# Kernel optimization log

Measured on AMD Instinct MI355X. Metric: run time of the kernel, lower is better.

## Reference

```python
import jax, jax.numpy as jnp
import numpy as np

N_QUBITS = 8
DIM = 2 ** N_QUBITS  # 256
N_CYCLES = 4
BATCH = 8192

# ---- gate matrices (work for scalar or batched [B] angles) ----

def _rz(t):
    e0 = jnp.exp(-0.5j * t.astype(jnp.complex64))
    e1 = jnp.exp(0.5j * t.astype(jnp.complex64))
    z = jnp.zeros_like(e0)
    return jnp.stack([jnp.stack([e0, z], -1), jnp.stack([z, e1], -1)], -2)


def _ry(t):
    c = jnp.cos(t / 2)
    s = jnp.sin(t / 2)
    m = jnp.stack([jnp.stack([c, -s], -1), jnp.stack([s, c], -1)], -2)
    return m.astype(jnp.complex64)


def _u3(t, p, l):
    ct = jnp.cos(t / 2).astype(jnp.complex64)
    st = jnp.sin(t / 2).astype(jnp.complex64)
    ep = jnp.exp(1j * p.astype(jnp.complex64))
    el = jnp.exp(1j * l.astype(jnp.complex64))
    return jnp.stack([jnp.stack([ct, -el * st], -1),
                      jnp.stack([ep * st, ep * el * ct], -1)], -2)

# ---- state-vector gate application (wire 0 = most significant, torchquantum convention) ----

def apply_1q(psi, U, w):
    B = psi.shape[0]
    p = psi.reshape(B, 2 ** w, 2, -1)
    if U.ndim == 3:
        p = jnp.einsum('bij,bajc->baic', U, p)
    else:
        p = jnp.einsum('ij,bajc->baic', U, p)
    return p.reshape(B, DIM)


def apply_cnot(psi, c, t):
    p = psi.reshape((-1,) + (2,) * N_QUBITS)
    c_ax, t_ax = c + 1, t + 1
    p0 = jax.lax.index_in_dim(p, 0, c_ax, keepdims=True)
    p1 = jnp.flip(jax.lax.index_in_dim(p, 1, c_ax, keepdims=True), axis=t_ax)
    return jnp.concatenate([p0, p1], axis=c_ax).reshape(-1, DIM)


def expval_z(psi, w):
    pr = (psi.real ** 2 + psi.imag ** 2).reshape(psi.shape[0], 2 ** w, 2, -1)
    pr = pr.sum(axis=(1, 3))
    return pr[:, 0] - pr[:, 1]


def conv_block(psi, hi, lo, rza, rzb, rzc, rya, ryb):
    # rz(hi); cnot(hi,lo); rz(lo); ry(hi); cnot(lo,hi); ry(hi); cnot(hi,lo); rz(lo)
    psi = apply_1q(psi, _rz(rza), hi)
    psi = apply_cnot(psi, hi, lo)
    psi = apply_1q(psi, _rz(rzb), lo)
    psi = apply_1q(psi, _ry(rya), hi)
    psi = apply_cnot(psi, lo, hi)
    psi = apply_1q(psi, _ry(ryb), hi)
    psi = apply_cnot(psi, hi, lo)
    psi = apply_1q(psi, _rz(rzc), lo)
    return psi


def _forward(theta, phi, rz_angles, ry_angles, u3_params, w1, b1, w2, b2):
    B = theta.shape[0]
    psi = jnp.zeros((B, DIM), jnp.complex64).at[:, 0].set(1.0)
    # circuit builder (assumed): per cycle RY(theta), RZ(phi) on every wire + CNOT ring
    Ury = _ry(theta)  # [B,2,2]
    Urz = _rz(phi)
    for _ in range(N_CYCLES):
        for w in range(N_QUBITS):
            psi = apply_1q(psi, Ury, w)
        for w in range(N_QUBITS):
            psi = apply_1q(psi, Urz, w)
        for w in range(N_QUBITS):
            psi = apply_cnot(psi, w, (w + 1) % N_QUBITS)
    # conv layer 1: pairs (1,0),(3,2),(5,4),(7,6) using rz1-12, ry1-8
    for i, (hi, lo) in enumerate([(1, 0), (3, 2), (5, 4), (7, 6)]):
        psi = conv_block(psi, hi, lo, rz_angles[3 * i], rz_angles[3 * i + 1],
                         rz_angles[3 * i + 2], ry_angles[2 * i], ry_angles[2 * i + 1])
    # intermediate expvals on [0,2,4,6] are computed-and-discarded in the original (non-collapsing): no-op
    for j, w in enumerate([1, 3, 5, 7]):
        psi = apply_1q(psi, _u3(u3_params[j, 0], u3_params[j, 1], u3_params[j, 2]), w)
    # conv layer 2: pairs (3,1),(7,5),(5,3) using rz13-21, ry9-14
    for k, (hi, lo) in enumerate([(3, 1), (7, 5), (5, 3)]):
        i = 4 + k
        psi = conv_block(psi, hi, lo, rz_angles[3 * i], rz_angles[3 * i + 1],
                         rz_angles[3 * i + 2], ry_angles[2 * i], ry_angles[2 * i + 1])
    # discarded expvals on [1,5]: no-op
    psi = apply_1q(psi, _u3(u3_params[4, 0], u3_params[4, 1], u3_params[4, 2]), 3)
    psi = apply_1q(psi, _u3(u3_params[5, 0], u3_params[5, 1], u3_params[5, 2]), 7)
    x = jnp.stack([expval_z(psi, 3), expval_z(psi, 7)], axis=-1)  # [B,2] real
    h = jnp.tanh(x @ w1.T + b1)
    y = h @ w2.T + b2
    return jax.nn.sigmoid(y)  # [B,1]


def setup_inputs() -> dict:
    key = jax.random.key(0)
    ks = jax.random.split(key, 9)
    return {
        'theta': jax.random.normal(ks[0], (BATCH,), jnp.float32),
        'phi': jax.random.normal(ks[1], (BATCH,), jnp.float32),
        'rz_angles': jax.random.normal(ks[2], (21,), jnp.float32),
        'ry_angles': jax.random.normal(ks[3], (14,), jnp.float32),
        'u3_params': jax.random.normal(ks[4], (6, 3), jnp.float32),
        'w1': jax.random.normal(ks[5], (10, 2), jnp.float32) * 0.5,
        'b1': jax.random.normal(ks[6], (10,), jnp.float32) * 0.1,
        'w2': jax.random.normal(ks[7], (1, 10), jnp.float32) * 0.3,
        'b2': jax.random.normal(ks[8], (1,), jnp.float32) * 0.1,
    }


def reference(theta, phi, rz_angles, ry_angles, u3_params, w1, b1, w2, b2):
    return _forward(theta, phi, rz_angles, ry_angles, u3_params, w1, b1, w2, b2)
```

## Files before the change

kernel.cpp:

```cpp
#include <hip/hip_runtime.h>
#include <math.h>


constexpr int NREG = 8;

typedef float v2f __attribute__((ext_vector_type(2)));

__device__ __forceinline__ v2f vfma(v2f a, v2f b, v2f c) {
  return __builtin_elementwise_fma(a, b, c);
}
__device__ __forceinline__ v2f splat(float x) { return (v2f){x, x}; }

template<int MASK>
__device__ __forceinline__ float lxor(float x) {
  int xi = __float_as_int(x);
  int r;
  if constexpr (MASK == 1)      r = __builtin_amdgcn_mov_dpp(xi, 0xB1, 0xF, 0xF, true);
  else if constexpr (MASK == 2) r = __builtin_amdgcn_mov_dpp(xi, 0x4E, 0xF, 0xF, true);
  else                          r = __builtin_amdgcn_ds_swizzle(xi, (MASK << 10) | 0x1F);
  return __int_as_float(r);
}

template<int MASK>
__device__ __forceinline__ v2f lxor2(v2f v) {
  v2f r;
  r.x = lxor<MASK>(v.x);
  r.y = lxor<MASK>(v.y);
  return r;
}

struct State {
  v2f a[NREG];
};

template<int P>
__device__ __forceinline__ void ry_gate(State& st, float c, float s, int L) {
  if constexpr (P <= 2) {
    constexpr int m = 1 << P;
    #pragma unroll
    for (int r0 = 0; r0 < NREG; ++r0) {
      if (r0 & m) continue;
      const int r1 = r0 | m;
      v2f a0 = st.a[r0], a1 = st.a[r1];
      st.a[r0] = vfma(splat(-s), a1, splat(c) * a0);
      st.a[r1] = vfma(splat( s), a0, splat(c) * a1);
    }
  } else {
    constexpr int m = 1 << (P - 3);
    float ss = ((L >> (P - 3)) & 1) ? s : -s;
    #pragma unroll
    for (int r = 0; r < NREG; ++r) {
      v2f b = lxor2<m>(st.a[r]);
      st.a[r] = vfma(splat(ss), b, splat(c) * st.a[r]);
    }
  }
}

template<int P>
__device__ __forceinline__ void rz_gate(State& st, float cz, float sz, int L) {
  if constexpr (P <= 2) {
    #pragma unroll
    for (int r = 0; r < NREG; ++r) {
      float sg = ((r >> P) & 1) ? sz : -sz;
      v2f v = st.a[r];
      st.a[r] = vfma((v2f){-sg, sg}, v.yx, splat(cz) * v);
    }
  } else {
    float sg = ((L >> (P - 3)) & 1) ? sz : -sz;
    #pragma unroll
    for (int r = 0; r < NREG; ++r) {
      v2f v = st.a[r];
      st.a[r] = vfma((v2f){-sg, sg}, v.yx, splat(cz) * v);
    }
  }
}

template<int PC, int PT>
__device__ __forceinline__ void cnot_gate(State& st, int L) {
  if constexpr (PT <= 2) {
    constexpr int mt = 1 << PT;
    if constexpr (PC <= 2) {
      constexpr int mc = 1 << PC;
      #pragma unroll
      for (int r0 = 0; r0 < NREG; ++r0) {
        if (!(r0 & mc) || (r0 & mt)) continue;
        const int r1 = r0 | mt;
        v2f t = st.a[r0]; st.a[r0] = st.a[r1]; st.a[r1] = t;
      }
    } else {
      bool cb = (L >> (PC - 3)) & 1;
      #pragma unroll
      for (int r0 = 0; r0 < NREG; ++r0) {
        if (r0 & mt) continue;
        const int r1 = r0 | mt;
        v2f a0 = st.a[r0], a1 = st.a[r1];
        st.a[r0] = cb ? a1 : a0;
        st.a[r1] = cb ? a0 : a1;
      }
    }
  } else {
    constexpr int mt = 1 << (PT - 3);
    if constexpr (PC <= 2) {
      constexpr int mc = 1 << PC;
      #pragma unroll
      for (int r = 0; r < NREG; ++r) {
        if (!(r & mc)) continue;
        st.a[r] = lxor2<mt>(st.a[r]);
      }
    } else {
      bool cb = (L >> (PC - 3)) & 1;
      #pragma unroll
      for (int r = 0; r < NREG; ++r) {
        v2f b = lxor2<mt>(st.a[r]);
        st.a[r] = cb ? b : st.a[r];
      }
    }
  }
}

__device__ __forceinline__ v2f cmac(v2f t, float ur, float ui, v2f v) {
  t = vfma(splat(ur), v, t);
  t = vfma((v2f){-ui, ui}, v.yx, t);
  return t;
}

template<int P>
__device__ __forceinline__ void u3_gate(State& st, const float* u, int L) {
  float u00r=u[0],u00i=u[1],u01r=u[2],u01i=u[3],u10r=u[4],u10i=u[5],u11r=u[6],u11i=u[7];
  if constexpr (P <= 2) {
    constexpr int m = 1 << P;
    #pragma unroll
    for (int r0 = 0; r0 < NREG; ++r0) {
      if (r0 & m) continue;
      const int r1 = r0 | m;
      v2f a0 = st.a[r0], a1 = st.a[r1];
      v2f t0 = splat(u00r) * a0;
      t0 = vfma((v2f){-u00i, u00i}, a0.yx, t0);
      t0 = cmac(t0, u01r, u01i, a1);
      v2f t1 = splat(u10r) * a0;
      t1 = vfma((v2f){-u10i, u10i}, a0.yx, t1);
      t1 = cmac(t1, u11r, u11i, a1);
      st.a[r0] = t0;
      st.a[r1] = t1;
    }
  } else {
    constexpr int m = 1 << (P - 3);
    bool b = (L >> (P - 3)) & 1;
    float xr = b ? u11r : u00r, xi = b ? u11i : u00i;
    float yr = b ? u10r : u01r, yi = b ? u10i : u01i;
    #pragma unroll
    for (int r = 0; r < NREG; ++r) {
      v2f p = lxor2<m>(st.a[r]);
      v2f v = st.a[r];
      v2f t = splat(xr) * v;
      t = vfma((v2f){-xi, xi}, v.yx, t);
      t = cmac(t, yr, yi, p);
      st.a[r] = t;
    }
  }
}

template<int PH, int PL>
__device__ __forceinline__ void conv_block(State& st, int L,
    float crza,float srza, float crzb,float srzb, float crzc,float srzc,
    float crya,float srya, float cryb,float sryb) {
  rz_gate<PH>(st, crza, srza, L);
  cnot_gate<PH, PL>(st, L);
  rz_gate<PL>(st, crzb, srzb, L);
  ry_gate<PH>(st, crya, srya, L);
  cnot_gate<PL, PH>(st, L);
  ry_gate<PH>(st, cryb, sryb, L);
  cnot_gate<PH, PL>(st, L);
  rz_gate<PL>(st, crzc, srzc, L);
}

__global__ __launch_bounds__(256, 4) void qcnn_kernel(
    const float* __restrict__ theta, const float* __restrict__ phi,
    const float* __restrict__ rz_a, const float* __restrict__ ry_a,
    const float* __restrict__ u3_p,
    const float* __restrict__ w1, const float* __restrict__ b1,
    const float* __restrict__ w2, const float* __restrict__ b2,
    float* __restrict__ out, int B) {
  __shared__ float s_rz[21][2];
  __shared__ float s_ry[14][2];
  __shared__ float s_u3[6][8];
  __shared__ float s_w1[20];
  __shared__ float s_b1[10];
  __shared__ float s_w2[10];
  __shared__ float s_b2[1];

  const int tid = threadIdx.x;
  if (tid < 21) {
    float s, c; sincosf(0.5f * rz_a[tid], &s, &c);
    s_rz[tid][0] = c; s_rz[tid][1] = s;
  } else if (tid >= 32 && tid < 46) {
    int j = tid - 32;
    float s, c; sincosf(0.5f * ry_a[j], &s, &c);
    s_ry[j][0] = c; s_ry[j][1] = s;
  } else if (tid >= 64 && tid < 70) {
    int j = tid - 64;
    float t = u3_p[3*j], p = u3_p[3*j+1], l = u3_p[3*j+2];
    float st_, ct, sp, cp, sl, cl;
    sincosf(0.5f*t, &st_, &ct);
    sincosf(p, &sp, &cp);
    sincosf(l, &sl, &cl);
    s_u3[j][0] = ct;       s_u3[j][1] = 0.f;
    s_u3[j][2] = -cl*st_;  s_u3[j][3] = -sl*st_;
    s_u3[j][4] = cp*st_;   s_u3[j][5] = sp*st_;
    float eplr = cp*cl - sp*sl, epli = sp*cl + cp*sl;
    s_u3[j][6] = eplr*ct;  s_u3[j][7] = epli*ct;
  } else if (tid >= 96 && tid < 116) {
    s_w1[tid - 96] = w1[tid - 96];
  } else if (tid >= 128 && tid < 138) {
    s_b1[tid - 128] = b1[tid - 128];
  } else if (tid >= 160 && tid < 170) {
    s_w2[tid - 160] = w2[tid - 160];
  } else if (tid == 192) {
    s_b2[0] = b2[0];
  }
  __syncthreads();

  const int L = tid & 31;
  const int g = (blockIdx.x * blockDim.x + tid) >> 5;
  if (g < B) {
    float th = theta[g], ph = phi[g];
    float cth, sth; sincosf(0.5f*th, &sth, &cth);
    float cph, sph; sincosf(0.5f*ph, &sph, &cph);

    State st;
    #pragma unroll
    for (int r = 0; r < NREG; ++r) st.a[r] = (v2f){0.f, 0.f};
    st.a[0].x = (L == 0) ? 1.f : 0.f;

    #pragma unroll 1
    for (int cyc = 0; cyc < 4; ++cyc) {
      ry_gate<7>(st, cth, sth, L);
      ry_gate<6>(st, cth, sth, L);
      ry_gate<5>(st, cth, sth, L);
      ry_gate<4>(st, cth, sth, L);
      ry_gate<3>(st, cth, sth, L);
      ry_gate<2>(st, cth, sth, L);
      ry_gate<1>(st, cth, sth, L);
      ry_gate<0>(st, cth, sth, L);
      rz_gate<7>(st, cph, sph, L);
      rz_gate<6>(st, cph, sph, L);
      rz_gate<5>(st, cph, sph, L);
      rz_gate<4>(st, cph, sph, L);
      rz_gate<3>(st, cph, sph, L);
      rz_gate<2>(st, cph, sph, L);
      rz_gate<1>(st, cph, sph, L);
      rz_gate<0>(st, cph, sph, L);
      cnot_gate<7,6>(st, L);
      cnot_gate<6,5>(st, L);
      cnot_gate<5,4>(st, L);
      cnot_gate<4,3>(st, L);
      cnot_gate<3,2>(st, L);
      cnot_gate<2,1>(st, L);
      cnot_gate<1,0>(st, L);
      cnot_gate<0,7>(st, L);
    }

    #define CONVB(PH, PL, i) conv_block<PH, PL>(st, L, \
        s_rz[3*(i)][0],   s_rz[3*(i)][1],   \
        s_rz[3*(i)+1][0], s_rz[3*(i)+1][1], \
        s_rz[3*(i)+2][0], s_rz[3*(i)+2][1], \
        s_ry[2*(i)][0],   s_ry[2*(i)][1],   \
        s_ry[2*(i)+1][0], s_ry[2*(i)+1][1])
    CONVB(6, 7, 0);
    CONVB(4, 5, 1);
    CONVB(2, 3, 2);
    CONVB(0, 1, 3);

    u3_gate<6>(st, s_u3[0], L);
    u3_gate<4>(st, s_u3[1], L);
    u3_gate<2>(st, s_u3[2], L);
    u3_gate<0>(st, s_u3[3], L);

    CONVB(4, 6, 4);
    CONVB(0, 2, 5);
    CONVB(2, 4, 6);
    #undef CONVB

    u3_gate<4>(st, s_u3[4], L);
    u3_gate<0>(st, s_u3[5], L);

    float s3 = 0.f, s7 = 0.f;
    #pragma unroll
    for (int r = 0; r < NREG; ++r) {
      v2f sq = st.a[r] * st.a[r];
      float p = sq.x + sq.y;
      s3 += p;
      s7 += (r & 1) ? -p : p;
    }
    if ((L >> 1) & 1) s3 = -s3;
    s3 += lxor<1>(s3);  s7 += lxor<1>(s7);
    s3 += lxor<2>(s3);  s7 += lxor<2>(s7);
    s3 += lxor<4>(s3);  s7 += lxor<4>(s7);
    s3 += lxor<8>(s3);  s7 += lxor<8>(s7);
    s3 += lxor<16>(s3); s7 += lxor<16>(s7);

    float y = s_b2[0];
    #pragma unroll
    for (int j = 0; j < 10; ++j) {
      float h = tanhf(fmaf(s3, s_w1[2*j], fmaf(s7, s_w1[2*j+1], s_b1[j])));
      y = fmaf(h, s_w2[j], y);
    }
    float res = 1.f / (1.f + expf(-y));
    if (L == 0) out[g] = res;
  }
}

extern "C" void kernel_launch(void* const* d_in, const int* in_sizes, int n_in,
                              void* d_out, int out_size, void* d_ws, size_t ws_size,
                              hipStream_t stream) {
  const float* theta = (const float*)d_in[0];
  const float* phi   = (const float*)d_in[1];
  const float* rz_a  = (const float*)d_in[2];
  const float* ry_a  = (const float*)d_in[3];
  const float* u3_p  = (const float*)d_in[4];
  const float* w1    = (const float*)d_in[5];
  const float* b1    = (const float*)d_in[6];
  const float* w2    = (const float*)d_in[7];
  const float* b2    = (const float*)d_in[8];
  float* out = (float*)d_out;
  const int B = in_sizes[0];
  const int threads = 256;
  const int blocks = (B * 32 + threads - 1) / threads;
  hipLaunchKernelGGL(qcnn_kernel, dim3(blocks), dim3(threads), 0, stream,
                     theta, phi, rz_a, ry_a, u3_p, w1, b1, w2, b2, out, B);
}
```

Measured before the change: 31.92 us.

## Process two batch elements per 32-lane group to raise ILP

Each 32-lane group now simulates two independent state vectors (two batch samples) interleaved in registers, halving the grid size and giving every gate two independent dependency chains. The aim is to hide DPP/swizzle and FMA latency and to amortize the per-group setup, parameter reads and reduction. In exchange register use doubles and launch bounds drop to 2 blocks per CU, which lowers occupancy and leaves fewer blocks to spread across CUs.

New measurement: 34.63 us. 1.08x slower.

```diff
diff --git a/kernel.cpp b/kernel.cpp
--- a/kernel.cpp
+++ b/kernel.cpp
@@ -29,54 +29,85 @@
   return r;
 }
 
-struct State {
-  v2f a[NREG];
+struct St2 {
+  v2f a[2][NREG];
 };
 
+
 template<int P>
-__device__ __forceinline__ void ry_gate(State& st, float c, float s, int L) {
+__device__ __forceinline__ void ry2(St2& st, float c0, float s0, float c1, float s1, int L) {
+  const float cc[2] = {c0, c1};
+  const float ss[2] = {s0, s1};
   if constexpr (P <= 2) {
     constexpr int m = 1 << P;
     #pragma unroll
     for (int r0 = 0; r0 < NREG; ++r0) {
       if (r0 & m) continue;
       const int r1 = r0 | m;
-      v2f a0 = st.a[r0], a1 = st.a[r1];
-      st.a[r0] = vfma(splat(-s), a1, splat(c) * a0);
-      st.a[r1] = vfma(splat( s), a0, splat(c) * a1);
+      #pragma unroll
+      for (int e = 0; e < 2; ++e) {
+        v2f a0 = st.a[e][r0], a1 = st.a[e][r1];
+        st.a[e][r0] = vfma(splat(-ss[e]), a1, splat(cc[e]) * a0);
+        st.a[e][r1] = vfma(splat( ss[e]), a0, splat(cc[e]) * a1);
+      }
     }
   } else {
     constexpr int m = 1 << (P - 3);
-    float ss = ((L >> (P - 3)) & 1) ? s : -s;
+    const bool bit = (L >> (P - 3)) & 1;
+    const float sg[2] = {bit ? s0 : -s0, bit ? s1 : -s1};
     #pragma unroll
     for (int r = 0; r < NREG; ++r) {
-      v2f b = lxor2<m>(st.a[r]);
-      st.a[r] = vfma(splat(ss), b, splat(c) * st.a[r]);
+      #pragma unroll
+      for (int e = 0; e < 2; ++e) {
+        v2f b = lxor2<m>(st.a[e][r]);
+        st.a[e][r] = vfma(splat(sg[e]), b, splat(cc[e]) * st.a[e][r]);
+      }
     }
   }
 }
 
 template<int P>
-__device__ __forceinline__ void rz_gate(State& st, float cz, float sz, int L) {
+__device__ __forceinline__ void rz2(St2& st, float c0, float s0, float c1, float s1, int L) {
+  const float cc[2] = {c0, c1};
+  const float ss[2] = {s0, s1};
   if constexpr (P <= 2) {
     #pragma unroll
     for (int r = 0; r < NREG; ++r) {
-      float sg = ((r >> P) & 1) ? sz : -sz;
-      v2f v = st.a[r];
-      st.a[r] = vfma((v2f){-sg, sg}, v.yx, splat(cz) * v);
+      const bool bit = (r >> P) & 1;
+      #pragma unroll
+      for (int e = 0; e < 2; ++e) {
+        float sg = bit ? ss[e] : -ss[e];
+        v2f v = st.a[e][r];
+        st.a[e][r] = vfma((v2f){-sg, sg}, v.yx, splat(cc[e]) * v);
+      }
     }
   } else {
-    float sg = ((L >> (P - 3)) & 1) ? sz : -sz;
+    const bool bit = (L >> (P - 3)) & 1;
+    const float sg[2] = {bit ? s0 : -s0, bit ? s1 : -s1};
     #pragma unroll
     for (int r = 0; r < NREG; ++r) {
-      v2f v = st.a[r];
-      st.a[r] = vfma((v2f){-sg, sg}, v.yx, splat(cz) * v);
-    }
-  }
+      #pragma unroll
+      for (int e = 0; e < 2; ++e) {
+        v2f v = st.a[e][r];
+        st.a[e][r] = vfma((v2f){-sg[e], sg[e]}, v.yx, splat(cc[e]) * v);
+      }
+    }
+  }
+}
+
+
+template<int P>
+__device__ __forceinline__ void ry_s(St2& st, float c, float s, int L) {
+  ry2<P>(st, c, s, c, s, L);
+}
+
+template<int P>
+__device__ __forceinline__ void rz_s(St2& st, float cz, float sz, int L) {
+  rz2<P>(st, cz, sz, cz, sz, L);
 }
 
 template<int PC, int PT>
-__device__ __forceinline__ void cnot_gate(State& st, int L) {
+__device__ __forceinline__ void cnot2(St2& st, int L) {
   if constexpr (PT <= 2) {
     constexpr int mt = 1 << PT;
     if constexpr (PC <= 2) {
@@ -85,17 +116,23 @@
       for (int r0 = 0; r0 < NREG; ++r0) {
         if (!(r0 & mc) || (r0 & mt)) continue;
         const int r1 = r0 | mt;
-        v2f t = st.a[r0]; st.a[r0] = st.a[r1]; st.a[r1] = t;
+        #pragma unroll
+        for (int e = 0; e < 2; ++e) {
+          v2f t = st.a[e][r0]; st.a[e][r0] = st.a[e][r1]; st.a[e][r1] = t;
+        }
       }
     } else {
-      bool cb = (L >> (PC - 3)) & 1;
+      const bool cb = (L >> (PC - 3)) & 1;
       #pragma unroll
       for (int r0 = 0; r0 < NREG; ++r0) {
         if (r0 & mt) continue;
         const int r1 = r0 | mt;
-        v2f a0 = st.a[r0], a1 = st.a[r1];
-        st.a[r0] = cb ? a1 : a0;
-        st.a[r1] = cb ? a0 : a1;
+        #pragma unroll
+        for (int e = 0; e < 2; ++e) {
+          v2f a0 = st.a[e][r0], a1 = st.a[e][r1];
+          st.a[e][r0] = cb ? a1 : a0;
+          st.a[e][r1] = cb ? a0 : a1;
+        }
       }
     }
   } else {
@@ -105,14 +142,18 @@
       #pragma unroll
       for (int r = 0; r < NREG; ++r) {
         if (!(r & mc)) continue;
-        st.a[r] = lxor2<mt>(st.a[r]);
+        #pragma unroll
+        for (int e = 0; e < 2; ++e) st.a[e][r] = lxor2<mt>(st.a[e][r]);
       }
     } else {
-      bool cb = (L >> (PC - 3)) & 1;
+      const bool cb = (L >> (PC - 3)) & 1;
       #pragma unroll
       for (int r = 0; r < NREG; ++r) {
-        v2f b = lxor2<mt>(st.a[r]);
-        st.a[r] = cb ? b : st.a[r];
+        #pragma unroll
+        for (int e = 0; e < 2; ++e) {
+          v2f b = lxor2<mt>(st.a[e][r]);
+          st.a[e][r] = cb ? b : st.a[e][r];
+        }
       }
     }
   }
@@ -125,7 +166,7 @@
 }
 
 template<int P>
-__device__ __forceinline__ void u3_gate(State& st, const float* u, int L) {
+__device__ __forceinline__ void u3_s(St2& st, const float* u, int L) {
   float u00r=u[0],u00i=u[1],u01r=u[2],u01i=u[3],u10r=u[4],u10i=u[5],u11r=u[6],u11i=u[7];
   if constexpr (P <= 2) {
     constexpr int m = 1 << P;
@@ -133,48 +174,54 @@
     for (int r0 = 0; r0 < NREG; ++r0) {
       if (r0 & m) continue;
       const int r1 = r0 | m;
-      v2f a0 = st.a[r0], a1 = st.a[r1];
-      v2f t0 = splat(u00r) * a0;
-      t0 = vfma((v2f){-u00i, u00i}, a0.yx, t0);
-      t0 = cmac(t0, u01r, u01i, a1);
-      v2f t1 = splat(u10r) * a0;
-      t1 = vfma((v2f){-u10i, u10i}, a0.yx, t1);
-      t1 = cmac(t1, u11r, u11i, a1);
-      st.a[r0] = t0;
-      st.a[r1] = t1;
+      #pragma unroll
+      for (int e = 0; e < 2; ++e) {
+        v2f a0 = st.a[e][r0], a1 = st.a[e][r1];
+        v2f t0 = splat(u00r) * a0;
+        t0 = vfma((v2f){-u00i, u00i}, a0.yx, t0);
+        t0 = cmac(t0, u01r, u01i, a1);
+        v2f t1 = splat(u10r) * a0;
+        t1 = vfma((v2f){-u10i, u10i}, a0.yx, t1);
+        t1 = cmac(t1, u11r, u11i, a1);
+        st.a[e][r0] = t0;
+        st.a[e][r1] = t1;
+      }
     }
   } else {
     constexpr int m = 1 << (P - 3);
-    bool b = (L >> (P - 3)) & 1;
-    float xr = b ? u11r : u00r, xi = b ? u11i : u00i;
-    float yr = b ? u10r : u01r, yi = b ? u10i : u01i;
+    const bool b = (L >> (P - 3)) & 1;
+    const float xr = b ? u11r : u00r, xi = b ? u11i : u00i;
+    const float yr = b ? u10r : u01r, yi = b ? u10i : u01i;
     #pragma unroll
     for (int r = 0; r < NREG; ++r) {
-      v2f p = lxor2<m>(st.a[r]);
-      v2f v = st.a[r];
-      v2f t = splat(xr) * v;
-      t = vfma((v2f){-xi, xi}, v.yx, t);
-      t = cmac(t, yr, yi, p);
-      st.a[r] = t;
+      #pragma unroll
+      for (int e = 0; e < 2; ++e) {
+        v2f p = lxor2<m>(st.a[e][r]);
+        v2f v = st.a[e][r];
+        v2f t = splat(xr) * v;
+        t = vfma((v2f){-xi, xi}, v.yx, t);
+        t = cmac(t, yr, yi, p);
+        st.a[e][r] = t;
+      }
     }
   }
 }
 
 template<int PH, int PL>
-__device__ __forceinline__ void conv_block(State& st, int L,
+__device__ __forceinline__ void conv_block(St2& st, int L,
     float crza,float srza, float crzb,float srzb, float crzc,float srzc,
     float crya,float srya, float cryb,float sryb) {
-  rz_gate<PH>(st, crza, srza, L);
-  cnot_gate<PH, PL>(st, L);
-  rz_gate<PL>(st, crzb, srzb, L);
-  ry_gate<PH>(st, crya, srya, L);
-  cnot_gate<PL, PH>(st, L);
-  ry_gate<PH>(st, cryb, sryb, L);
-  cnot_gate<PH, PL>(st, L);
-  rz_gate<PL>(st, crzc, srzc, L);
-}
-
-__global__ __launch_bounds__(256, 4) void qcnn_kernel(
+  rz_s<PH>(st, crza, srza, L);
+  cnot2<PH, PL>(st, L);
+  rz_s<PL>(st, crzb, srzb, L);
+  ry_s<PH>(st, crya, srya, L);
+  cnot2<PL, PH>(st, L);
+  ry_s<PH>(st, cryb, sryb, L);
+  cnot2<PH, PL>(st, L);
+  rz_s<PL>(st, crzc, srzc, L);
+}
+
+__global__ __launch_bounds__(256, 2) void qcnn_kernel(
     const float* __restrict__ theta, const float* __restrict__ phi,
     const float* __restrict__ rz_a, const float* __restrict__ ry_a,
     const float* __restrict__ u3_p,
@@ -221,43 +268,52 @@
   __syncthreads();
 
   const int L = tid & 31;
-  const int g = (blockIdx.x * blockDim.x + tid) >> 5;
-  if (g < B) {
-    float th = theta[g], ph = phi[g];
-    float cth, sth; sincosf(0.5f*th, &sth, &cth);
-    float cph, sph; sincosf(0.5f*ph, &sph, &cph);
-
-    State st;
-    #pragma unroll
-    for (int r = 0; r < NREG; ++r) st.a[r] = (v2f){0.f, 0.f};
-    st.a[0].x = (L == 0) ? 1.f : 0.f;
+  const int grp = (blockIdx.x * blockDim.x + tid) >> 5;
+  const int g0 = 2 * grp;
+  const int g1 = 2 * grp + 1;
+  if (g0 < B) {
+    const int g1r = (g1 < B) ? g1 : g0;
+    float th0 = theta[g0], ph0 = phi[g0];
+    float th1 = theta[g1r], ph1 = phi[g1r];
+    float cth0, sth0; sincosf(0.5f*th0, &sth0, &cth0);
+    float cth1, sth1; sincosf(0.5f*th1, &sth1, &cth1);
+    float cph0, sph0; sincosf(0.5f*ph0, &sph0, &cph0);
+    float cph1, sph1; sincosf(0.5f*ph1, &sph1, &cph1);
+
+    St2 st;
+    #pragma unroll
+    for (int e = 0; e < 2; ++e)
+      #pragma unroll
+      for (int r = 0; r < NREG; ++r) st.a[e][r] = (v2f){0.f, 0.f};
+    st.a[0][0].x = (L == 0) ? 1.f : 0.f;
+    st.a[1][0].x = (L == 0) ? 1.f : 0.f;
 
     #pragma unroll 1
     for (int cyc = 0; cyc < 4; ++cyc) {
-      ry_gate<7>(st, cth, sth, L);
-      ry_gate<6>(st, cth, sth, L);
-      ry_gate<5>(st, cth, sth, L);
-      ry_gate<4>(st, cth, sth, L);
-      ry_gate<3>(st, cth, sth, L);
-      ry_gate<2>(st, cth, sth, L);
-      ry_gate<1>(st, cth, sth, L);
-      ry_gate<0>(st, cth, sth, L);
-      rz_gate<7>(st, cph, sph, L);
-      rz_gate<6>(st, cph, sph, L);
-      rz_gate<5>(st, cph, sph, L);
-      rz_gate<4>(st, cph, sph, L);
-      rz_gate<3>(st, cph, sph, L);
-      rz_gate<2>(st, cph, sph, L);
-      rz_gate<1>(st, cph, sph, L);
-      rz_gate<0>(st, cph, sph, L);
-      cnot_gate<7,6>(st, L);
-      cnot_gate<6,5>(st, L);
-      cnot_gate<5,4>(st, L);
-      cnot_gate<4,3>(st, L);
-      cnot_gate<3,2>(st, L);
-      cnot_gate<2,1>(st, L);
-      cnot_gate<1,0>(st, L);
-      cnot_gate<0,7>(st, L);
+      ry2<7>(st, cth0, sth0, cth1, sth1, L);
+      ry2<6>(st, cth0, sth0, cth1, sth1, L);
+      ry2<5>(st, cth0, sth0, cth1, sth1, L);
+      ry2<4>(st, cth0, sth0, cth1, sth1, L);
+      ry2<3>(st, cth0, sth0, cth1, sth1, L);
+      ry2<2>(st, cth0, sth0, cth1, sth1, L);
+      ry2<1>(st, cth0, sth0, cth1, sth1, L);
+      ry2<0>(st, cth0, sth0, cth1, sth1, L);
+      rz2<7>(st, cph0, sph0, cph1, sph1, L);
+      rz2<6>(st, cph0, sph0, cph1, sph1, L);
+      rz2<5>(st, cph0, sph0, cph1, sph1, L);
+      rz2<4>(st, cph0, sph0, cph1, sph1, L);
+      rz2<3>(st, cph0, sph0, cph1, sph1, L);
+      rz2<2>(st, cph0, sph0, cph1, sph1, L);
+      rz2<1>(st, cph0, sph0, cph1, sph1, L);
+      rz2<0>(st, cph0, sph0, cph1, sph1, L);
+      cnot2<7,6>(st, L);
+      cnot2<6,5>(st, L);
+      cnot2<5,4>(st, L);
+      cnot2<4,3>(st, L);
+      cnot2<3,2>(st, L);
+      cnot2<2,1>(st, L);
+      cnot2<1,0>(st, L);
+      cnot2<0,7>(st, L);
     }
 
     #define CONVB(PH, PL, i) conv_block<PH, PL>(st, L, \
@@ -271,42 +327,56 @@
     CONVB(2, 3, 2);
     CONVB(0, 1, 3);
 
-    u3_gate<6>(st, s_u3[0], L);
-    u3_gate<4>(st, s_u3[1], L);
-    u3_gate<2>(st, s_u3[2], L);
-    u3_gate<0>(st, s_u3[3], L);
+    u3_s<6>(st, s_u3[0], L);
+    u3_s<4>(st, s_u3[1], L);
+    u3_s<2>(st, s_u3[2], L);
+    u3_s<0>(st, s_u3[3], L);
 
     CONVB(4, 6, 4);
     CONVB(0, 2, 5);
     CONVB(2, 4, 6);
     #undef CONVB
 
-    u3_gate<4>(st, s_u3[4], L);
-    u3_gate<0>(st, s_u3[5], L);
-
-    float s3 = 0.f, s7 = 0.f;
+    u3_s<4>(st, s_u3[4], L);
+    u3_s<0>(st, s_u3[5], L);
+
+    float s3[2] = {0.f, 0.f}, s7[2] = {0.f, 0.f};
     #pragma unroll
     for (int r = 0; r < NREG; ++r) {
-      v2f sq = st.a[r] * st.a[r];
-      float p = sq.x + sq.y;
-      s3 += p;
-      s7 += (r & 1) ? -p : p;
-    }
-    if ((L >> 1) & 1) s3 = -s3;
-    s3 += lxor<1>(s3);  s7 += lxor<1>(s7);
-    s3 += lxor<2>(s3);  s7 += lxor<2>(s7);
-    s3 += lxor<4>(s3);  s7 += lxor<4>(s7);
-    s3 += lxor<8>(s3);  s7 += lxor<8>(s7);
-    s3 += lxor<16>(s3); s7 += lxor<16>(s7);
-
-    float y = s_b2[0];
-    #pragma unroll
-    for (int j = 0; j < 10; ++j) {
-      float h = tanhf(fmaf(s3, s_w1[2*j], fmaf(s7, s_w1[2*j+1], s_b1[j])));
-      y = fmaf(h, s_w2[j], y);
-    }
-    float res = 1.f / (1.f + expf(-y));
-    if (L == 0) out[g] = res;
+      #pragma unroll
+      for (int e = 0; e < 2; ++e) {
+        v2f sq = st.a[e][r] * st.a[e][r];
+        float p = sq.x + sq.y;
+        s3[e] += p;
+        s7[e] += (r & 1) ? -p : p;
+      }
+    }
+    const bool neg3 = (L >> 1) & 1;
+    #pragma unroll
+    for (int e = 0; e < 2; ++e) {
+      if (neg3) s3[e] = -s3[e];
+      s3[e] += lxor<1>(s3[e]);  s7[e] += lxor<1>(s7[e]);
+      s3[e] += lxor<2>(s3[e]);  s7[e] += lxor<2>(s7[e]);
+      s3[e] += lxor<4>(s3[e]);  s7[e] += lxor<4>(s7[e]);
+      s3[e] += lxor<8>(s3[e]);  s7[e] += lxor<8>(s7[e]);
+      s3[e] += lxor<16>(s3[e]); s7[e] += lxor<16>(s7[e]);
+    }
+
+    float res[2];
+    #pragma unroll
+    for (int e = 0; e < 2; ++e) {
+      float y = s_b2[0];
+      #pragma unroll
+      for (int j = 0; j < 10; ++j) {
+        float h = tanhf(fmaf(s3[e], s_w1[2*j], fmaf(s7[e], s_w1[2*j+1], s_b1[j])));
+        y = fmaf(h, s_w2[j], y);
+      }
+      res[e] = 1.f / (1.f + expf(-y));
+    }
+    if (L == 0) {
+      out[g0] = res[0];
+      if (g1 < B) out[g1] = res[1];
+    }
   }
 }
 
@@ -324,8 +394,9 @@
   const float* b2    = (const float*)d_in[8];
   float* out = (float*)d_out;
   const int B = in_sizes[0];
+  const int ngrp = (B + 1) / 2;
   const int threads = 256;
-  const int blocks = (B * 32 + threads - 1) / threads;
+  const int blocks = (ngrp * 32 + threads - 1) / threads;
   hipLaunchKernelGGL(qcnn_kernel, dim3(blocks), dim3(threads), 0, stream,
                      theta, phi, rz_a, ry_a, u3_p, w1, b1, w2, b2, out, B);
 }
```

## Fuse each conv block plus trailing U3 into a precomputed 4x4 two-qubit unitary

Applied to the files above, without the earlier changes.

The gate-angle-only conv blocks and the U3 gates that follow them are collapsed into seven dense complex 4x4 matrices, built once per thread block by a few threads and kept in shared memory. Each sample's state then gets one two-qubit matrix application per block, using lane shuffles or register pairs depending on where the qubits live, in place of eight separate gates. This cuts the number of gate passes and shuffles in the tail of the circuit. In exchange, each 4x4 application does more complex multiply-adds and reads more values from shared memory.

Measured after the change: 39.31 us. 23.1% more time.

```diff
diff --git a/kernel.cpp b/kernel.cpp
--- a/kernel.cpp
+++ b/kernel.cpp
@@ -32,6 +32,7 @@
 struct State {
   v2f a[NREG];
 };
+
 
 template<int P>
 __device__ __forceinline__ void ry_gate(State& st, float c, float s, int L) {
@@ -118,60 +119,160 @@
   }
 }
 
-__device__ __forceinline__ v2f cmac(v2f t, float ur, float ui, v2f v) {
-  t = vfma(splat(ur), v, t);
-  t = vfma((v2f){-ui, ui}, v.yx, t);
+__device__ __forceinline__ v2f cmac(v2f t, v2f u, v2f v) {
+  t = vfma(splat(u.x), v, t);
+  t = vfma((v2f){-u.y, u.y}, v.yx, t);
   return t;
 }
 
-template<int P>
-__device__ __forceinline__ void u3_gate(State& st, const float* u, int L) {
-  float u00r=u[0],u00i=u[1],u01r=u[2],u01i=u[3],u10r=u[4],u10i=u[5],u11r=u[6],u11i=u[7];
-  if constexpr (P <= 2) {
-    constexpr int m = 1 << P;
-    #pragma unroll
-    for (int r0 = 0; r0 < NREG; ++r0) {
-      if (r0 & m) continue;
-      const int r1 = r0 | m;
-      v2f a0 = st.a[r0], a1 = st.a[r1];
-      v2f t0 = splat(u00r) * a0;
-      t0 = vfma((v2f){-u00i, u00i}, a0.yx, t0);
-      t0 = cmac(t0, u01r, u01i, a1);
-      v2f t1 = splat(u10r) * a0;
-      t1 = vfma((v2f){-u10i, u10i}, a0.yx, t1);
-      t1 = cmac(t1, u11r, u11i, a1);
-      st.a[r0] = t0;
-      st.a[r1] = t1;
-    }
+__device__ __forceinline__ v2f ld2(const float* p) {
+  return (v2f){p[0], p[1]};
+}
+
+
+template<int MH, int ML>
+__device__ __forceinline__ void apply_G_ll(State& st, const float* g, int L) {
+  const int bh = (L & MH) ? 1 : 0;
+  const int bl = (L & ML) ? 1 : 0;
+  const int row = (bh << 1) | bl;
+  const float* gr = g + row * 8;
+  const v2f cS = ld2(gr + 2 * row);
+  const v2f cL = ld2(gr + 2 * (row ^ 1));
+  const v2f cH = ld2(gr + 2 * (row ^ 2));
+  const v2f cB = ld2(gr + 2 * (row ^ 3));
+  #pragma unroll
+  for (int r = 0; r < NREG; ++r) {
+    v2f v = st.a[r];
+    v2f pl = lxor2<ML>(v);
+    v2f ph = lxor2<MH>(v);
+    v2f pb = lxor2<MH | ML>(v);
+    v2f t = (v2f){0.f, 0.f};
+    t = cmac(t, cS, v);
+    t = cmac(t, cL, pl);
+    t = cmac(t, cH, ph);
+    t = cmac(t, cB, pb);
+    st.a[r] = t;
+  }
+}
+
+template<int MHR, int MLR>
+__device__ __forceinline__ void apply_G_rr(State& st, const float* g) {
+  #pragma unroll
+  for (int base = 0; base < NREG; ++base) {
+    if (base & (MHR | MLR)) continue;
+    v2f in0 = st.a[base];
+    v2f in1 = st.a[base | MLR];
+    v2f in2 = st.a[base | MHR];
+    v2f in3 = st.a[base | MHR | MLR];
+    #pragma unroll
+    for (int i = 0; i < 4; ++i) {
+      v2f t = (v2f){0.f, 0.f};
+      t = cmac(t, ld2(g + i * 8 + 0), in0);
+      t = cmac(t, ld2(g + i * 8 + 2), in1);
+      t = cmac(t, ld2(g + i * 8 + 4), in2);
+      t = cmac(t, ld2(g + i * 8 + 6), in3);
+      st.a[base | ((i >> 1) ? MHR : 0) | ((i & 1) ? MLR : 0)] = (i == 0) ? t : t;
+      if (i == 0) st.a[base] = t;
+      else if (i == 1) st.a[base | MLR] = t;
+      else if (i == 2) st.a[base | MHR] = t;
+      else st.a[base | MHR | MLR] = t;
+    }
+  }
+}
+
+template<int MREG, int ML>
+__device__ __forceinline__ void apply_G_mx(State& st, const float* g, int L) {
+  const int bl = (L & ML) ? 1 : 0;
+  const int r0w = bl;
+  const int r1w = 2 + bl;
+  const float* g0 = g + r0w * 8;
+  const float* g1 = g + r1w * 8;
+  const v2f c0S = ld2(g0 + 2 * r0w),       c0L = ld2(g0 + 2 * (r0w ^ 1));
+  const v2f c0H = ld2(g0 + 2 * (r0w ^ 2)), c0B = ld2(g0 + 2 * (r0w ^ 3));
+  const v2f c1S = ld2(g1 + 2 * r1w),       c1L = ld2(g1 + 2 * (r1w ^ 1));
+  const v2f c1H = ld2(g1 + 2 * (r1w ^ 2)), c1B = ld2(g1 + 2 * (r1w ^ 3));
+  v2f x[NREG];
+  #pragma unroll
+  for (int r = 0; r < NREG; ++r) x[r] = lxor2<ML>(st.a[r]);
+  v2f o[NREG];
+  #pragma unroll
+  for (int r = 0; r < NREG; ++r) {
+    v2f t = (v2f){0.f, 0.f};
+    if (r & MREG) {
+      t = cmac(t, c1S, st.a[r]);
+      t = cmac(t, c1L, x[r]);
+      t = cmac(t, c1H, st.a[r ^ MREG]);
+      t = cmac(t, c1B, x[r ^ MREG]);
+    } else {
+      t = cmac(t, c0S, st.a[r]);
+      t = cmac(t, c0L, x[r]);
+      t = cmac(t, c0H, st.a[r ^ MREG]);
+      t = cmac(t, c0B, x[r ^ MREG]);
+    }
+    o[r] = t;
+  }
+  #pragma unroll
+  for (int r = 0; r < NREG; ++r) st.a[r] = o[r];
+}
+
+
+__device__ __forceinline__ void b_phase(float* cr, float* ci, int i, float pc, float ps) {
+  float r = cr[i] * pc - ci[i] * ps;
+  float m = cr[i] * ps + ci[i] * pc;
+  cr[i] = r; ci[i] = m;
+}
+__device__ __forceinline__ void b_rz_hi(float* cr, float* ci, float t) {
+  float s, c; sincosf(0.5f * t, &s, &c);
+  b_phase(cr, ci, 0, c, -s); b_phase(cr, ci, 1, c, -s);
+  b_phase(cr, ci, 2, c,  s); b_phase(cr, ci, 3, c,  s);
+}
+__device__ __forceinline__ void b_rz_lo(float* cr, float* ci, float t) {
+  float s, c; sincosf(0.5f * t, &s, &c);
+  b_phase(cr, ci, 0, c, -s); b_phase(cr, ci, 2, c, -s);
+  b_phase(cr, ci, 1, c,  s); b_phase(cr, ci, 3, c,  s);
+}
+__device__ __forceinline__ void b_ry_hi(float* cr, float* ci, float t) {
+  float s, c; sincosf(0.5f * t, &s, &c);
+  #pragma unroll
+  for (int lo = 0; lo < 2; ++lo) {
+    int i0 = lo, i1 = 2 + lo;
+    float n0r = c * cr[i0] - s * cr[i1], n0i = c * ci[i0] - s * ci[i1];
+    float n1r = s * cr[i0] + c * cr[i1], n1i = s * ci[i0] + c * ci[i1];
+    cr[i0] = n0r; ci[i0] = n0i; cr[i1] = n1r; ci[i1] = n1i;
+  }
+}
+__device__ __forceinline__ void b_swap(float* cr, float* ci, int i, int j) {
+  float t;
+  t = cr[i]; cr[i] = cr[j]; cr[j] = t;
+  t = ci[i]; ci[i] = ci[j]; ci[j] = t;
+}
+__device__ __forceinline__ void b_u2(float* cr, float* ci, int i0, int i1,
+    float u00r, float u00i, float u01r, float u01i,
+    float u10r, float u10i, float u11r, float u11i) {
+  float v0r = cr[i0], v0i = ci[i0], v1r = cr[i1], v1i = ci[i1];
+  cr[i0] = u00r*v0r - u00i*v0i + u01r*v1r - u01i*v1i;
+  ci[i0] = u00r*v0i + u00i*v0r + u01r*v1i + u01i*v1r;
+  cr[i1] = u10r*v0r - u10i*v0i + u11r*v1r - u11i*v1i;
+  ci[i1] = u10r*v0i + u10i*v0r + u11r*v1i + u11i*v1r;
+}
+__device__ __forceinline__ void b_u3(float* cr, float* ci, bool on_hi,
+                                     float t, float p, float l) {
+  float st_, ct, sp, cp, sl, cl;
+  sincosf(0.5f * t, &st_, &ct);
+  sincosf(p, &sp, &cp);
+  sincosf(l, &sl, &cl);
+  float u00r = ct,        u00i = 0.f;
+  float u01r = -cl * st_, u01i = -sl * st_;
+  float u10r = cp * st_,  u10i = sp * st_;
+  float eplr = cp * cl - sp * sl, epli = sp * cl + cp * sl;
+  float u11r = eplr * ct, u11i = epli * ct;
+  if (on_hi) {
+    b_u2(cr, ci, 0, 2, u00r,u00i,u01r,u01i,u10r,u10i,u11r,u11i);
+    b_u2(cr, ci, 1, 3, u00r,u00i,u01r,u01i,u10r,u10i,u11r,u11i);
   } else {
-    constexpr int m = 1 << (P - 3);
-    bool b = (L >> (P - 3)) & 1;
-    float xr = b ? u11r : u00r, xi = b ? u11i : u00i;
-    float yr = b ? u10r : u01r, yi = b ? u10i : u01i;
-    #pragma unroll
-    for (int r = 0; r < NREG; ++r) {
-      v2f p = lxor2<m>(st.a[r]);
-      v2f v = st.a[r];
-      v2f t = splat(xr) * v;
-      t = vfma((v2f){-xi, xi}, v.yx, t);
-      t = cmac(t, yr, yi, p);
-      st.a[r] = t;
-    }
-  }
-}
-
-template<int PH, int PL>
-__device__ __forceinline__ void conv_block(State& st, int L,
-    float crza,float srza, float crzb,float srzb, float crzc,float srzc,
-    float crya,float srya, float cryb,float sryb) {
-  rz_gate<PH>(st, crza, srza, L);
-  cnot_gate<PH, PL>(st, L);
-  rz_gate<PL>(st, crzb, srzb, L);
-  ry_gate<PH>(st, crya, srya, L);
-  cnot_gate<PL, PH>(st, L);
-  ry_gate<PH>(st, cryb, sryb, L);
-  cnot_gate<PH, PL>(st, L);
-  rz_gate<PL>(st, crzc, srzc, L);
+    b_u2(cr, ci, 0, 1, u00r,u00i,u01r,u01i,u10r,u10i,u11r,u11i);
+    b_u2(cr, ci, 2, 3, u00r,u00i,u01r,u01i,u10r,u10i,u11r,u11i);
+  }
 }
 
 __global__ __launch_bounds__(256, 4) void qcnn_kernel(
@@ -181,34 +282,37 @@
     const float* __restrict__ w1, const float* __restrict__ b1,
     const float* __restrict__ w2, const float* __restrict__ b2,
     float* __restrict__ out, int B) {
-  __shared__ float s_rz[21][2];
-  __shared__ float s_ry[14][2];
-  __shared__ float s_u3[6][8];
+  __shared__ float sG[7 * 32] __attribute__((aligned(16)));
   __shared__ float s_w1[20];
   __shared__ float s_b1[10];
   __shared__ float s_w2[10];
   __shared__ float s_b2[1];
 
   const int tid = threadIdx.x;
-  if (tid < 21) {
-    float s, c; sincosf(0.5f * rz_a[tid], &s, &c);
-    s_rz[tid][0] = c; s_rz[tid][1] = s;
-  } else if (tid >= 32 && tid < 46) {
-    int j = tid - 32;
-    float s, c; sincosf(0.5f * ry_a[j], &s, &c);
-    s_ry[j][0] = c; s_ry[j][1] = s;
-  } else if (tid >= 64 && tid < 70) {
-    int j = tid - 64;
-    float t = u3_p[3*j], p = u3_p[3*j+1], l = u3_p[3*j+2];
-    float st_, ct, sp, cp, sl, cl;
-    sincosf(0.5f*t, &st_, &ct);
-    sincosf(p, &sp, &cp);
-    sincosf(l, &sl, &cl);
-    s_u3[j][0] = ct;       s_u3[j][1] = 0.f;
-    s_u3[j][2] = -cl*st_;  s_u3[j][3] = -sl*st_;
-    s_u3[j][4] = cp*st_;   s_u3[j][5] = sp*st_;
-    float eplr = cp*cl - sp*sl, epli = sp*cl + cp*sl;
-    s_u3[j][6] = eplr*ct;  s_u3[j][7] = epli*ct;
+  if (tid < 7) {
+    const int t = tid;
+    #pragma unroll
+    for (int j = 0; j < 4; ++j) {
+      float cr[4] = {0.f, 0.f, 0.f, 0.f};
+      float ci[4] = {0.f, 0.f, 0.f, 0.f};
+      cr[j] = 1.f;
+      b_rz_hi(cr, ci, rz_a[3 * t]);
+      b_swap(cr, ci, 2, 3);
+      b_rz_lo(cr, ci, rz_a[3 * t + 1]);
+      b_ry_hi(cr, ci, ry_a[2 * t]);
+      b_swap(cr, ci, 1, 3);
+      b_ry_hi(cr, ci, ry_a[2 * t + 1]);
+      b_swap(cr, ci, 2, 3);
+      b_rz_lo(cr, ci, rz_a[3 * t + 2]);
+      if (t < 4)       b_u3(cr, ci, true,  u3_p[3*t],  u3_p[3*t+1],  u3_p[3*t+2]);
+      else if (t == 5) b_u3(cr, ci, true,  u3_p[15],   u3_p[16],     u3_p[17]);
+      else if (t == 6) b_u3(cr, ci, false, u3_p[12],   u3_p[13],     u3_p[14]);
+      #pragma unroll
+      for (int i = 0; i < 4; ++i) {
+        sG[t * 32 + i * 8 + j * 2]     = cr[i];
+        sG[t * 32 + i * 8 + j * 2 + 1] = ci[i];
+      }
+    }
   } else if (tid >= 96 && tid < 116) {
     s_w1[tid - 96] = w1[tid - 96];
   } else if (tid >= 128 && tid < 138) {
@@ -224,8 +328,8 @@
   const int g = (blockIdx.x * blockDim.x + tid) >> 5;
   if (g < B) {
     float th = theta[g], ph = phi[g];
-    float cth, sth; sincosf(0.5f*th, &sth, &cth);
-    float cph, sph; sincosf(0.5f*ph, &sph, &cph);
+    float cth, sth; sincosf(0.5f * th, &sth, &cth);
+    float cph, sph; sincosf(0.5f * ph, &sph, &cph);
 
     State st;
     #pragma unroll
@@ -260,29 +364,13 @@
       cnot_gate<0,7>(st, L);
     }
 
-    #define CONVB(PH, PL, i) conv_block<PH, PL>(st, L, \
-        s_rz[3*(i)][0],   s_rz[3*(i)][1],   \
-        s_rz[3*(i)+1][0], s_rz[3*(i)+1][1], \
-        s_rz[3*(i)+2][0], s_rz[3*(i)+2][1], \
-        s_ry[2*(i)][0],   s_ry[2*(i)][1],   \
-        s_ry[2*(i)+1][0], s_ry[2*(i)+1][1])
-    CONVB(6, 7, 0);
-    CONVB(4, 5, 1);
-    CONVB(2, 3, 2);
-    CONVB(0, 1, 3);
-
-    u3_gate<6>(st, s_u3[0], L);
-    u3_gate<4>(st, s_u3[1], L);
-    u3_gate<2>(st, s_u3[2], L);
-    u3_gate<0>(st, s_u3[3], L);
-
-    CONVB(4, 6, 4);
-    CONVB(0, 2, 5);
-    CONVB(2, 4, 6);
-    #undef CONVB
-
-    u3_gate<4>(st, s_u3[4], L);
-    u3_gate<0>(st, s_u3[5], L);
+    apply_G_ll<8, 16>(st, sG + 0 * 32, L);
+    apply_G_ll<2, 4>(st, sG + 1 * 32, L);
+    apply_G_mx<4, 1>(st, sG + 2 * 32, L);
+    apply_G_rr<1, 2>(st, sG + 3 * 32);
+    apply_G_ll<2, 8>(st, sG + 4 * 32, L);
+    apply_G_rr<1, 4>(st, sG + 5 * 32);
+    apply_G_mx<4, 2>(st, sG + 6 * 32, L);
 
     float s3 = 0.f, s7 = 0.f;
     #pragma unroll
```
